# Optimization experiments

Hardware: AMD Instinct MI355X
Metric: run time of the kernel (lower is better)

The kernel has to match this reference:

```python
import jax, jax.numpy as jnp
import numpy as np

N_NODES, N_EDGES, C_IN = 50000, 320000, 512
DIMS = [C_IN, 2048, 1024, 512, 256, 128]


def setup_inputs() -> dict:
    key = jax.random.key(0)
    ks = jax.random.split(key, 2 + 2 * 5)
    inp = {
        "x": jax.random.normal(ks[0], (N_NODES, C_IN), jnp.float32),
        "edge_index": jax.random.randint(ks[1], (2, N_EDGES), 0, N_NODES, dtype=jnp.int64),
    }
    for i in range(5):
        fan_in = DIMS[i]
        inp[f"W{i+1}"] = jax.random.normal(ks[2 + 2 * i], (DIMS[i], DIMS[i + 1]), jnp.float32) / np.float32(np.sqrt(fan_in))
        inp[f"b{i+1}"] = jnp.zeros((DIMS[i + 1],), jnp.float32)
    return inp


def _gcn_layer(h, W, b, src, dst, dinv, n_nodes):
    # PyG GCNConv: h' = D^{-1/2} (A + I) D^{-1/2} (h W) + b, deg includes self-loop
    h = h @ W                                  # [N, out]
    norm = (dinv[src] * dinv[dst])[:, None]    # per-edge normalization
    agg = jax.ops.segment_sum(h[src] * norm, dst, num_segments=n_nodes)
    agg = agg + h * (dinv * dinv)[:, None]     # self-loop contribution
    return agg + b


def reference(x, edge_index, W1, b1, W2, b2, W3, b3, W4, b4, W5, b5):
    n = x.shape[0]
    src, dst = edge_index[0], edge_index[1]
    # in-degree (at dst) + 1 for self-loop, as in PyG gcn_norm
    deg = jax.ops.segment_sum(jnp.ones(src.shape[0], x.dtype), dst, num_segments=n) + 1.0
    dinv = jax.lax.rsqrt(deg)
    # dropout is identity in eval mode (training=False)
    h = jax.nn.relu(_gcn_layer(x, W1, b1, src, dst, dinv, n))
    h = jax.nn.relu(_gcn_layer(h, W2, b2, src, dst, dinv, n))
    h = jax.nn.relu(_gcn_layer(h, W3, b3, src, dst, dinv, n))
    h = jax.nn.relu(_gcn_layer(h, W4, b4, src, dst, dinv, n))
    return _gcn_layer(h, W5, b5, src, dst, dinv, n)
```

## Files before the change

kernel.cpp:

```cpp
#include <hip/hip_runtime.h>
#include <hip/hip_bf16.h>
#include <stdint.h>

#define N_NODES 50000
#define N_EDGES 320000
#define MP 50048

typedef __hip_bfloat16 bf16_t;
typedef __attribute__((ext_vector_type(8))) short short8;
typedef __attribute__((ext_vector_type(4))) float floatx4;

__global__ void detect_kernel(const int* __restrict__ ei, int* __restrict__ flag) {
    int tid = threadIdx.x;
    int v = ei[2 * tid + 1];
    unsigned long long b = __ballot(v != 0);
    if (tid == 0) *flag = (b == 0ull) ? 1 : 0;
}

__device__ __forceinline__ int load_edge(const int* ei, int row, int e, int is64) {
    long pos = (long)row * N_EDGES + e;
    return is64 ? ei[2 * pos] : ei[pos];
}

#define CB 1250
#define XB 25024
#define WB 14976

__global__ __launch_bounds__(256)
void preproc_kernel(const int* __restrict__ ei, const int* __restrict__ flag,
                    int* __restrict__ counts,
                    const float* __restrict__ x, bf16_t* __restrict__ xb,
                    const float* __restrict__ W1, const float* __restrict__ W2,
                    const float* __restrict__ W3, const float* __restrict__ W4,
                    const float* __restrict__ W5,
                    bf16_t* __restrict__ wt1, bf16_t* __restrict__ wt2,
                    bf16_t* __restrict__ wt3, bf16_t* __restrict__ wt4,
                    bf16_t* __restrict__ wt5) {
    int bid = blockIdx.x;
    int tid = threadIdx.x;
    if (bid < CB) {
        int e = bid * 256 + tid;
        if (e < N_EDGES) {
            int d = load_edge(ei, 1, e, *flag);
            atomicAdd(&counts[d], 1);
        }
    } else if (bid < CB + XB) {
        long idx = ((long)(bid - CB) * 256 + tid) * 4;
        union { bf16_t h[4]; uint2 u; } o;
        long row = idx >> 9;
        if (row < N_NODES) {
            float4 v = *(const float4*)(x + idx);
            o.h[0] = __float2bfloat16(v.x);
            o.h[1] = __float2bfloat16(v.y);
            o.h[2] = __float2bfloat16(v.z);
            o.h[3] = __float2bfloat16(v.w);
        } else {
            o.u = make_uint2(0u, 0u);
        }
        *(uint2*)(xb + idx) = o.u;
    } else {
        long idx = (long)(bid - CB - XB) * 256 + tid;
        const float* Ws; bf16_t* Wd; int K, Nn; long off;
        if      (idx < 1048576) { Ws = W1; Wd = wt1; K = 512;  Nn = 2048; off = 0; }
        else if (idx < 3145728) { Ws = W2; Wd = wt2; K = 2048; Nn = 1024; off = 1048576; }
        else if (idx < 3670016) { Ws = W3; Wd = wt3; K = 1024; Nn = 512;  off = 3145728; }
        else if (idx < 3801088) { Ws = W4; Wd = wt4; K = 512;  Nn = 256;  off = 3670016; }
        else if (idx < 3833856) { Ws = W5; Wd = wt5; K = 256;  Nn = 128;  off = 3801088; }
        else return;
        long i = idx - off;
        int nn = (int)(i & (Nn - 1));
        int kk = (int)(i >> __builtin_ctz(Nn));
        Wd[(size_t)nn * K + kk] = __float2bfloat16(Ws[i]);
    }
}

__global__ __launch_bounds__(1024)
void scan_kernel(const int* __restrict__ counts, int* __restrict__ rowptr,
                 int* __restrict__ cursor, float* __restrict__ dinv,
                 float* __restrict__ selfw) {
    __shared__ int wsum[16];
    __shared__ int base_s;
    int tid  = threadIdx.x;
    int lane = tid & 63;
    int wv   = tid >> 6;
    if (tid == 0) base_s = 0;
    __syncthreads();
    for (int start = 0; start < N_NODES; start += 1024) {
        int i = start + tid;
        int v = (i < N_NODES) ? counts[i] : 0;
        int s = v;
#pragma unroll
        for (int off = 1; off < 64; off <<= 1) {
            int t = __shfl_up(s, off, 64);
            if (lane >= off) s += t;
        }
        if (lane == 63) wsum[wv] = s;
        __syncthreads();
        if (wv == 0 && lane < 16) {
            int t = wsum[lane];
#pragma unroll
            for (int off = 1; off < 16; off <<= 1) {
                int u = __shfl_up(t, off, 64);
                if (lane >= off) t += u;
            }
            wsum[lane] = t;
        }
        __syncthreads();
        int wbase = (wv == 0) ? 0 : wsum[wv - 1];
        int incl  = s + wbase;
        int base  = base_s;
        if (i < N_NODES) {
            int excl = base + incl - v;
            rowptr[i] = excl;
            cursor[i] = excl;
            float di = rsqrtf((float)v + 1.0f);
            dinv[i] = di;
            selfw[i] = di * di;
        }
        __syncthreads();
        if (tid == 1023) base_s = base + incl;
        __syncthreads();
    }
    if (tid == 0) rowptr[N_NODES] = N_EDGES;
}

__global__ void fill_kernel(const int* __restrict__ ei, const int* __restrict__ flag,
                            int* __restrict__ cursor, const float* __restrict__ dinv,
                            int* __restrict__ esrc, float* __restrict__ ewt) {
    int e = blockIdx.x * 256 + threadIdx.x;
    if (e < N_EDGES) {
        int is64 = *flag;
        int s = load_edge(ei, 0, e, is64);
        int d = load_edge(ei, 1, e, is64);
        int p = atomicAdd(&cursor[d], 1);
        esrc[p] = s;
        ewt[p]  = dinv[s] * dinv[d];
    }
}

#define BM 128
#define BN 128
#define BK 64

__device__ __forceinline__ void stage16(const bf16_t* g, bf16_t* l) {
    __builtin_amdgcn_global_load_lds(
        (const __attribute__((address_space(1))) void*)g,
        (__attribute__((address_space(3))) void*)l, 16, 0, 0);
}

__global__ __launch_bounds__(256)
void gemm_bf16(const bf16_t* __restrict__ A, const bf16_t* __restrict__ Bt,
               bf16_t* __restrict__ C, int K, int Nn,
               const float* __restrict__ bias, int relu, int nx, int ny) {
    int id   = blockIdx.x;
    int xcd  = id & 7;
    int slot = id >> 3;
    int y    = (slot / nx) * 8 + xcd;
    int xt   = slot % nx;
    if (y >= ny) return;

    __shared__ __align__(16) bf16_t ldsA[BM * BK];
    __shared__ __align__(16) bf16_t ldsB[BN * BK];

    int tid  = threadIdx.x;
    int lane = tid & 63;
    int wave = tid >> 6;
    int m15  = lane & 15;
    int quad = lane >> 4;
    int wm = (wave & 1) * 64;
    int wn = (wave >> 1) * 64;
    long bm0 = (long)y * BM;
    long bn0 = (long)xt * BN;

    floatx4 acc[4][4] = {};

    int rb   = tid >> 3;
    int cole = ((tid & 7) ^ (rb & 7)) * 8;
    const bf16_t* pa = A  + (bm0 + rb) * (long)K + cole;
    const bf16_t* pb = Bt + (bn0 + rb) * (long)K + cole;
    bf16_t* la = ldsA + tid * 8;
    bf16_t* lb = ldsB + tid * 8;
    const long step32 = 32 * (long)K;

    int fx   = lane & 7;
    int blk0 = ((0 + quad) ^ fx) * 8;
    int blk1 = ((4 + quad) ^ fx) * 8;
    int rowA = (wm + m15) * BK;
    int rowB = (wn + m15) * BK;

    for (int k0 = 0; k0 < K; k0 += BK) {
#pragma unroll
        for (int it = 0; it < 4; ++it) {
            stage16(pa + it * step32, la + it * 2048);
            stage16(pb + it * step32, lb + it * 2048);
        }
        pa += BK;
        pb += BK;
        __syncthreads();
#pragma unroll
        for (int kk = 0; kk < 2; ++kk) {
            int blk = kk ? blk1 : blk0;
            short8 af[4], bfr[4];
#pragma unroll
            for (int i = 0; i < 4; ++i)
                af[i] = *(const short8*)(&ldsA[rowA + i * (16 * BK) + blk]);
#pragma unroll
            for (int j = 0; j < 4; ++j)
                bfr[j] = *(const short8*)(&ldsB[rowB + j * (16 * BK) + blk]);
#pragma unroll
            for (int i = 0; i < 4; ++i)
#pragma unroll
                for (int j = 0; j < 4; ++j)
                    acc[i][j] = __builtin_amdgcn_mfma_f32_16x16x32_bf16(af[i], bfr[j], acc[i][j], 0, 0, 0);
        }
        __syncthreads();
    }

#pragma unroll
    for (int i = 0; i < 4; ++i) {
#pragma unroll
        for (int j = 0; j < 4; ++j) {
            long row0 = bm0 + wm + i * 16 + quad * 4;
            long col  = bn0 + wn + j * 16 + m15;
            float bv = bias ? bias[col] : 0.f;
#pragma unroll
            for (int r = 0; r < 4; ++r) {
                float v = acc[i][j][r] + bv;
                if (relu) v = fmaxf(v, 0.f);
                C[(row0 + r) * (long)Nn + col] = __float2bfloat16(v);
            }
        }
    }
}

__device__ __forceinline__ void unpack8(uint4 v, float* f) {
    uint32_t u[4] = {v.x, v.y, v.z, v.w};
#pragma unroll
    for (int i = 0; i < 4; ++i) {
        f[2 * i]     = __uint_as_float(u[i] << 16);
        f[2 * i + 1] = __uint_as_float(u[i] & 0xffff0000u);
    }
}

__global__ __launch_bounds__(256)
void agg_kernel(const bf16_t* __restrict__ hW, const int* __restrict__ rowptr,
                const int* __restrict__ esrc, const float* __restrict__ ewt,
                const float* __restrict__ selfw,
                const float* __restrict__ bias, bf16_t* __restrict__ outb,
                float* __restrict__ outf, int Nn, int chunks, int npw, int nsh,
                int relu, int rows) {
    int wave = threadIdx.x >> 6;
    int lane = threadIdx.x & 63;
    long unit = (long)blockIdx.x * 4 + wave;
    int n, c0;
    if (npw > 1) {
        int l8 = lane * 8;
        n  = (int)(unit * npw + (l8 >> nsh));
        c0 = l8 & (Nn - 1);
    } else {
        n  = (int)(unit / chunks);
        c0 = (int)(unit % chunks) * 512 + lane * 8;
    }
    if (n >= rows || c0 >= Nn) return;

    if (n >= N_NODES) {
        if (outb) *(uint4*)(outb + (size_t)n * Nn + c0) = make_uint4(0, 0, 0, 0);
        return;
    }

    int r0 = rowptr[n], r1 = rowptr[n + 1];
    float acc[8] = {};

    for (int e = r0; e < r1; e += 4) {
        int e1 = (e + 1 < r1) ? e + 1 : e;
        int e2 = (e + 2 < r1) ? e + 2 : e;
        int e3 = (e + 3 < r1) ? e + 3 : e;
        int s0 = esrc[e], s1 = esrc[e1], s2 = esrc[e2], s3 = esrc[e3];
        float w0 = ewt[e];
        float w1 = (e + 1 < r1) ? ewt[e1] : 0.f;
        float w2 = (e + 2 < r1) ? ewt[e2] : 0.f;
        float w3 = (e + 3 < r1) ? ewt[e3] : 0.f;
        uint4 v0 = *(const uint4*)(hW + (size_t)s0 * Nn + c0);
        uint4 v1 = *(const uint4*)(hW + (size_t)s1 * Nn + c0);
        uint4 v2 = *(const uint4*)(hW + (size_t)s2 * Nn + c0);
        uint4 v3 = *(const uint4*)(hW + (size_t)s3 * Nn + c0);
        float f0[8], f1[8], f2[8], f3[8];
        unpack8(v0, f0); unpack8(v1, f1); unpack8(v2, f2); unpack8(v3, f3);
#pragma unroll
        for (int j = 0; j < 8; ++j)
            acc[j] += f0[j] * w0 + f1[j] * w1 + f2[j] * w2 + f3[j] * w3;
    }

    {
        uint4 v = *(const uint4*)(hW + (size_t)n * Nn + c0);
        float fv[8]; unpack8(v, fv);
        float w = selfw[n];
#pragma unroll
        for (int j = 0; j < 8; ++j) acc[j] += fv[j] * w;
    }
    if (bias) {
#pragma unroll
        for (int j = 0; j < 8; ++j) acc[j] += bias[c0 + j];
    }
    if (relu) {
#pragma unroll
        for (int j = 0; j < 8; ++j) acc[j] = fmaxf(acc[j], 0.f);
    }
    if (outf) {
        *(float4*)(outf + (size_t)n * Nn + c0)     = make_float4(acc[0], acc[1], acc[2], acc[3]);
        *(float4*)(outf + (size_t)n * Nn + c0 + 4) = make_float4(acc[4], acc[5], acc[6], acc[7]);
    } else {
        union { bf16_t h[8]; uint4 u; } o;
#pragma unroll
        for (int j = 0; j < 8; ++j) o.h[j] = __float2bfloat16(acc[j]);
        *(uint4*)(outb + (size_t)n * Nn + c0) = o.u;
    }
}

extern "C" void kernel_launch(void* const* d_in, const int* in_sizes, int n_in,
                              void* d_out, int out_size, void* d_ws, size_t ws_size,
                              hipStream_t stream) {
    (void)in_sizes; (void)n_in; (void)out_size; (void)ws_size;
    const float* x  = (const float*)d_in[0];
    const int*   ei = (const int*)d_in[1];
    const float* W[5] = {(const float*)d_in[2], (const float*)d_in[4], (const float*)d_in[6],
                         (const float*)d_in[8], (const float*)d_in[10]};
    const float* B[5] = {(const float*)d_in[3], (const float*)d_in[5], (const float*)d_in[7],
                         (const float*)d_in[9], (const float*)d_in[11]};
    static const int dims[6] = {512, 2048, 1024, 512, 256, 128};

    const size_t SZ_A = (size_t)MP * 512 * 2;
    const size_t SZ_B = (size_t)MP * 512 * 2;
    const size_t SZ_C = (size_t)MP * 2048 * 2;
    char* base = (char*)d_ws;
    bf16_t* regA = (bf16_t*)base;
    bf16_t* regB = (bf16_t*)(base + SZ_A);
    bf16_t* regC = (bf16_t*)(base + SZ_A + SZ_B);
    char* p = base + SZ_A + SZ_B + SZ_C;
    auto take = [&](size_t bytes) { char* r = p; p += (bytes + 255) & ~(size_t)255; return r; };
    bf16_t* wt[5];
    for (int i = 0; i < 5; ++i) wt[i] = (bf16_t*)take((size_t)dims[i] * dims[i + 1] * 2);
    int*   counts = (int*)take((size_t)N_NODES * 4);
    int*   rowptr = (int*)take((size_t)(N_NODES + 1) * 4);
    int*   cursor = (int*)take((size_t)N_NODES * 4);
    int*   esrc   = (int*)take((size_t)N_EDGES * 4);
    float* ewt    = (float*)take((size_t)N_EDGES * 4);
    float* dinv   = (float*)take((size_t)N_NODES * 4);
    float* selfw  = (float*)take((size_t)N_NODES * 4);
    int*   eflag  = (int*)take(256);

    detect_kernel<<<1, 64, 0, stream>>>(ei, eflag);
    hipMemsetAsync(counts, 0, (size_t)N_NODES * 4, stream);
    bf16_t* xb = regA;
    preproc_kernel<<<CB + XB + WB, 256, 0, stream>>>(ei, eflag, counts, x, xb,
                                                     W[0], W[1], W[2], W[3], W[4],
                                                     wt[0], wt[1], wt[2], wt[3], wt[4]);
    scan_kernel<<<1, 1024, 0, stream>>>(counts, rowptr, cursor, dinv, selfw);
    fill_kernel<<<(N_EDGES + 255) / 256, 256, 0, stream>>>(ei, eflag, cursor, dinv, esrc, ewt);

    auto launch_gemm = [&](const bf16_t* a, const bf16_t* bt, bf16_t* c,
                           int K, int Nn, const float* bias, int relu) {
        int nx = Nn / BN;
        int ny = MP / BM;
        int blocks = nx * (((ny + 7) / 8) * 8);
        gemm_bf16<<<blocks, 256, 0, stream>>>(a, bt, c, K, Nn, bias, relu, nx, ny);
    };

    auto launch_agg = [&](const bf16_t* hw, const float* bias, bf16_t* outb,
                          float* outf, int Nn, int relu, int rows) {
        int chunks = Nn > 512 ? Nn / 512 : 1;
        int npw    = Nn < 512 ? 512 / Nn : 1;
        int nsh    = 31 - __builtin_clz(Nn);
        long units = (long)((rows + npw - 1) / npw) * chunks;
        int blocks = (int)((units + 3) / 4);
        agg_kernel<<<blocks, 256, 0, stream>>>(hw, rowptr, esrc, ewt, selfw, bias,
                                               outb, outf, Nn, chunks, npw, nsh, relu, rows);
    };

    bf16_t* g1 = regB;
    bf16_t* h1 = regC;
    launch_agg(xb, nullptr, g1, nullptr, 512, 0, MP);
    launch_gemm(g1, wt[0], h1, 512, 2048, B[0], 1);

    bf16_t* hwbuf[4] = {regA, regA, regA, regA};
    bf16_t* hbuf[3]  = {regC, regB, regB};
    const bf16_t* hin = h1;
    for (int l = 1; l < 5; ++l) {
        int K = dims[l], Nn = dims[l + 1];
        bf16_t* hw = hwbuf[l - 1];
        launch_gemm(hin, wt[l], hw, K, Nn, nullptr, 0);
        if (l < 4) {
            bf16_t* hn = hbuf[l - 1];
            launch_agg(hw, B[l], hn, nullptr, Nn, 1, MP);
            hin = hn;
        } else {
            launch_agg(hw, B[l], nullptr, (float*)d_out, Nn, 0, N_NODES);
        }
    }
}
```

Measured before the change: 1.107 ms.

## Warp-specialize GEMM with producer waves and double-buffered LDS pipeline

Adds two producer waves per GEMM block that stage A/B tiles into a two-stage LDS ring via global_load_lds, while four consumer waves run MFMA. Per-stage ready/done counters in shared memory, polled with sleep, replace the block-wide barriers. The intent is to overlap global loads with compute, which the previous single-buffer loop with two __syncthreads per step serialized. In exchange, LDS use doubles to 64KB per block, which lowers occupancy, and the spin-wait polling adds overhead and relies on the LDS atomic ordering being correct.

```diff
diff --git a/kernel.cpp b/kernel.cpp
--- a/kernel.cpp
+++ b/kernel.cpp
@@ -141,6 +141,7 @@
 #define BM 128
 #define BN 128
 #define BK 64
+#define NSTAGE 2
 
 __device__ __forceinline__ void stage16(const bf16_t* g, bf16_t* l) {
     __builtin_amdgcn_global_load_lds(
@@ -148,7 +149,7 @@
         (__attribute__((address_space(3))) void*)l, 16, 0, 0);
 }
 
-__global__ __launch_bounds__(256)
+__global__ __launch_bounds__(384)
 void gemm_bf16(const bf16_t* __restrict__ A, const bf16_t* __restrict__ Bt,
                bf16_t* __restrict__ C, int K, int Nn,
                const float* __restrict__ bias, int relu, int nx, int ny) {
@@ -159,28 +160,49 @@
     int xt   = slot % nx;
     if (y >= ny) return;
 
-    __shared__ __align__(16) bf16_t ldsA[BM * BK];
-    __shared__ __align__(16) bf16_t ldsB[BN * BK];
+    __shared__ __align__(16) bf16_t lds[NSTAGE * 16384];
+    __shared__ int ready[NSTAGE];
+    __shared__ int done[NSTAGE];
 
     int tid  = threadIdx.x;
     int lane = tid & 63;
     int wave = tid >> 6;
+    long bm0 = (long)y * BM;
+    long bn0 = (long)xt * BN;
+    int iters = K >> 6;
+
+    if (tid < NSTAGE) { ready[tid] = 0; done[tid] = 0; }
+    __syncthreads();
+
+    if (wave >= 4) {
+        int p = wave - 4;
+        bf16_t* sa = lds + p * 16384;
+        bf16_t* sb = sa + 8192;
+        for (int it = p; it < iters; it += NSTAGE) {
+            int u = it >> 1;
+            while (__atomic_load_n(&done[p], __ATOMIC_ACQUIRE) < 4 * u)
+                __builtin_amdgcn_s_sleep(1);
+            int k0 = it << 6;
+#pragma unroll
+            for (int j = 0; j < 16; ++j) {
+                int f   = j * 64 + lane;
+                int row = f >> 3;
+                int blk = ((f & 7) ^ (row & 7)) * 8;
+                stage16(A  + (bm0 + row) * (long)K + k0 + blk, sa + f * 8);
+                stage16(Bt + (bn0 + row) * (long)K + k0 + blk, sb + f * 8);
+            }
+            asm volatile("s_waitcnt vmcnt(0)" ::: "memory");
+            __atomic_store_n(&ready[p], it + 1, __ATOMIC_RELEASE);
+        }
+        return;
+    }
+
     int m15  = lane & 15;
     int quad = lane >> 4;
     int wm = (wave & 1) * 64;
     int wn = (wave >> 1) * 64;
-    long bm0 = (long)y * BM;
-    long bn0 = (long)xt * BN;
 
     floatx4 acc[4][4] = {};
-
-    int rb   = tid >> 3;
-    int cole = ((tid & 7) ^ (rb & 7)) * 8;
-    const bf16_t* pa = A  + (bm0 + rb) * (long)K + cole;
-    const bf16_t* pb = Bt + (bn0 + rb) * (long)K + cole;
-    bf16_t* la = ldsA + tid * 8;
-    bf16_t* lb = ldsB + tid * 8;
-    const long step32 = 32 * (long)K;
 
     int fx   = lane & 7;
     int blk0 = ((0 + quad) ^ fx) * 8;
@@ -188,32 +210,30 @@
     int rowA = (wm + m15) * BK;
     int rowB = (wn + m15) * BK;
 
-    for (int k0 = 0; k0 < K; k0 += BK) {
-#pragma unroll
-        for (int it = 0; it < 4; ++it) {
-            stage16(pa + it * step32, la + it * 2048);
-            stage16(pb + it * step32, lb + it * 2048);
-        }
-        pa += BK;
-        pb += BK;
-        __syncthreads();
+    for (int it = 0; it < iters; ++it) {
+        int s = it & 1;
+        while (__atomic_load_n(&ready[s], __ATOMIC_ACQUIRE) < it + 1)
+            __builtin_amdgcn_s_sleep(1);
+        const bf16_t* sa = lds + s * 16384;
+        const bf16_t* sb = sa + 8192;
 #pragma unroll
         for (int kk = 0; kk < 2; ++kk) {
             int blk = kk ? blk1 : blk0;
             short8 af[4], bfr[4];
 #pragma unroll
             for (int i = 0; i < 4; ++i)
-                af[i] = *(const short8*)(&ldsA[rowA + i * (16 * BK) + blk]);
+                af[i] = *(const short8*)(&sa[rowA + i * (16 * BK) + blk]);
 #pragma unroll
             for (int j = 0; j < 4; ++j)
-                bfr[j] = *(const short8*)(&ldsB[rowB + j * (16 * BK) + blk]);
+                bfr[j] = *(const short8*)(&sb[rowB + j * (16 * BK) + blk]);
 #pragma unroll
             for (int i = 0; i < 4; ++i)
 #pragma unroll
                 for (int j = 0; j < 4; ++j)
                     acc[i][j] = __builtin_amdgcn_mfma_f32_16x16x32_bf16(af[i], bfr[j], acc[i][j], 0, 0, 0);
         }
-        __syncthreads();
+        if (lane == 0)
+            __atomic_fetch_add(&done[s], 1, __ATOMIC_RELEASE);
     }
 
 #pragma unroll
@@ -363,7 +383,7 @@
         int nx = Nn / BN;
         int ny = MP / BM;
         int blocks = nx * (((ny + 7) / 8) * 8);
-        gemm_bf16<<<blocks, 256, 0, stream>>>(a, bt, c, K, Nn, bias, relu, nx, ny);
+        gemm_bf16<<<blocks, 384, 0, stream>>>(a, bt, c, K, Nn, bias, relu, nx, ny);
     };
 
     auto launch_agg = [&](const bf16_t* hw, const float* bias, bf16_t* outb,
```

Result: slower. 1.300 ms (+17.4%).
